# Kernel optimization log

Hardware: AMD Instinct MI355X
Metric: run time of the kernel (lower is better)

## Reference

```python
import jax, jax.numpy as jnp
import numpy as np

N = 65536      # n query/support points
NN = 34        # neighbors per point
K = 15         # kernel points
IN_F = 64
OUT_F = 64
RADIUS = 2.5
KP_EXTENT_CFG = 1.0
DENSITY = 5.0
EXTENT = KP_EXTENT_CFG * RADIUS / DENSITY  # effective KP_extent = 0.5
BN_EPS = 1e-6
LRELU_SLOPE = 0.1
POINT_DIM = 4  # modulated=True -> 3 offset dims + 1 modulation per kernel point


def make_kernel_points():
    # Deterministic stand-in for the precomputed kernel dispositions loaded
    # from disk in KPConv (fixed='center': first point at origin). Points lie
    # inside a ball of radius 1.5 * extent.
    rng = np.random.RandomState(42)
    kp = rng.normal(size=(K, 3))
    kp /= np.linalg.norm(kp, axis=1, keepdims=True)
    kp *= rng.uniform(0.3, 1.0, size=(K, 1))
    kp[0] = 0.0
    return jnp.asarray(kp * (1.5 * EXTENT), dtype=jnp.float32)


def setup_inputs() -> dict:
    key = jax.random.key(0)
    ks = jax.random.split(key, 8)
    query_points = jax.random.uniform(ks[0], (N, 3), dtype=jnp.float32)
    support_points = jax.random.uniform(ks[1], (N, 3), dtype=jnp.float32)
    neighbors_indices = jax.random.randint(ks[2], (N, NN), 0, N, dtype=jnp.int32)
    features = jax.random.normal(ks[3], (N, IN_F), dtype=jnp.float32)
    # weight_variable: truncated normal with std sqrt(2/size[-1])
    weight = jax.random.truncated_normal(ks[4], -2.0, 2.0, (K, IN_F, OUT_F), jnp.float32) * np.sqrt(2.0 / OUT_F)
    off_dim = POINT_DIM * K
    offset_weight = jax.random.truncated_normal(ks[5], -2.0, 2.0, (K, IN_F, off_dim), jnp.float32) * np.sqrt(2.0 / off_dim)
    offset_bias = jnp.zeros((off_dim,), jnp.float32)
    bn_gamma = jnp.ones((OUT_F,), jnp.float32)
    bn_beta = jnp.zeros((OUT_F,), jnp.float32)
    kernel_points = make_kernel_points()
    return dict(query_points=query_points, support_points=support_points,
                neighbors_indices=neighbors_indices, features=features,
                weight=weight, offset_weight=offset_weight, offset_bias=offset_bias,
                bn_gamma=bn_gamma, bn_beta=bn_beta, kernel_points=kernel_points)


def _influence(sq_dist):
    # KP_influence='linear': relu(1 - d / extent)
    return jax.nn.relu(1.0 - jnp.sqrt(sq_dist) / EXTENT)


def reference(query_points, support_points, neighbors_indices, features,
              weight, offset_weight, offset_bias, bn_gamma, bn_beta, kernel_points):
    n = query_points.shape[0]
    # Shadow point (far away) / shadow feature (zeros) appended at index n0
    supp_pad = jnp.concatenate([support_points, jnp.full((1, 3), 1e6, jnp.float32)], 0)
    feat_pad = jnp.concatenate([features, jnp.zeros((1, IN_F), jnp.float32)], 0)

    neigh_pts = supp_pad[neighbors_indices] - query_points[:, None, :]   # [n,nn,3]
    neigh_feats = feat_pad[neighbors_indices]                            # [n,nn,in]

    # ---- rigid KPConv producing per-point offsets (+ modulations) ----
    sq0 = jnp.sum((neigh_pts[:, :, None, :] - kernel_points[None, None]) ** 2, -1)  # [n,nn,K]
    w0 = _influence(sq0)
    wf0 = jnp.einsum('nak,nac->nkc', w0, neigh_feats)                    # [n,K,in]
    f0 = jnp.einsum('nkc,kcd->nd', wf0, offset_weight) + offset_bias     # [n,4K]
    offsets = f0[:, :3 * K].reshape(n, K, 3) * EXTENT                    # rescale to layer extent
    modulations = 2.0 * jax.nn.sigmoid(f0[:, 3 * K:])                    # [n,K]

    # ---- deformable KPConv ----
    def_kp = kernel_points[None] + offsets                               # [n,K,3]
    sq = jnp.sum((neigh_pts[:, :, None, :] - def_kp[:, None, :, :]) ** 2, -1)  # [n,nn,K]
    w = _influence(sq)                                                   # aggregation_mode='sum'
    wf = jnp.einsum('nak,nac->nkc', w, neigh_feats) * modulations[:, :, None]
    x = jnp.einsum('nkc,kco->no', wf, weight)                            # [n,out]

    # BatchNorm1d (training-mode batch stats, eps=1e-6) + LeakyReLU(0.1)
    mean = x.mean(0)
    var = x.var(0)
    x = (x - mean) * jax.lax.rsqrt(var + BN_EPS) * bn_gamma + bn_beta
    return jnp.where(x >= 0, x, LRELU_SLOPE * x)
```

## Files before the change

kernel.cpp:

```cpp
#include <hip/hip_runtime.h>
#include <math.h>

#define NPTS 65536

using half8   = __attribute__((ext_vector_type(8))) _Float16;
using half4   = __attribute__((ext_vector_type(4))) _Float16;
using floatx4 = __attribute__((ext_vector_type(4))) float;

__global__ __launch_bounds__(256) void k_prep(
    const float* __restrict__ ow, const float* __restrict__ w,
    const float* __restrict__ feat,
    _Float16* __restrict__ owt, _Float16* __restrict__ wt,
    _Float16* __restrict__ featH, float* __restrict__ stats)
{
  int b = blockIdx.x;
  if (b < 64) {
    __shared__ float tile[256][9];
    int mat = b >> 5, bb = b & 31;
    int kcb = bb & 3, db = bb >> 2;
    int t = threadIdx.x;
    int kc = kcb * 256 + t;
    int c = kc >> 4, k = kc & 15;
    const float* src = mat ? w : ow;
    int dmax = mat ? 64 : 60;
    #pragma unroll
    for (int di = 0; di < 8; ++di) {
      int d = db * 8 + di;
      float v = 0.f;
      if (k < 15 && d < dmax) v = src[(k * 64 + c) * dmax + d];
      tile[t][di] = v;
    }
    __syncthreads();
    _Float16* dst = mat ? wt : owt;
    int k2 = t >> 5, lo = t & 31;
    #pragma unroll
    for (int di = 0; di < 8; ++di) {
      int d = db * 8 + di;
      int wv = d >> 4, mm = d & 15;
      dst[((wv * 4 + kcb) * 8 + k2) * 512 + mm * 32 + lo] = (_Float16)tile[t][di];
    }
    if (b == 0 && t < 128) stats[t] = 0.f;
  } else {
    int j = (b - 64) * 256 + threadIdx.x;
    float4 f = ((const float4*)feat)[j];
    half4 h = {(_Float16)f.x, (_Float16)f.y, (_Float16)f.z, (_Float16)f.w};
    ((half4*)featH)[j] = h;
  }
}

__global__ __launch_bounds__(256, 4) void k_fused(
    const float* __restrict__ query, const float* __restrict__ support,
    const int* __restrict__ nidx, const _Float16* __restrict__ featH,
    const float* __restrict__ kpts, const float* __restrict__ obias,
    const _Float16* __restrict__ owt, const _Float16* __restrict__ wt,
    float* __restrict__ outx, float* __restrict__ stats)
{
  __shared__ float                  npx[16][34], npy[16][34], npz[16][34];
  __shared__ unsigned short         sidx[16][34];
  __shared__ __align__(16) _Float16 fT[4][64 * 32];
  __shared__ unsigned int           fx2s[16][64];
  __shared__ __align__(16) _Float16 wfh[16 * 264];
  __shared__ float                  dk[16][60];

  const int tid  = threadIdx.x;
  const int wave = tid >> 6, lane = tid & 63;
  const int quad = lane >> 4, mm = lane & 15;
  const int base = blockIdx.x * 16;
  _Float16* fTw = fT[wave];
  unsigned int* fTw32 = (unsigned int*)fTw;
  const floatx4 fz = {0.f, 0.f, 0.f, 0.f};
  const int me = (mm < 15) ? mm : 14;
  const int mmw = (mm & 6) | ((mm & 1) << 3) | ((mm >> 3) & 1);

  for (int s = tid; s < 544; s += 256) {
    int pt = s / 34, a = s - pt * 34;
    int n = base + pt;
    int id = nidx[n * 34 + a];
    npx[pt][a] = support[id * 3 + 0] - query[n * 3 + 0];
    npy[pt][a] = support[id * 3 + 1] - query[n * 3 + 1];
    npz[pt][a] = support[id * 3 + 2] - query[n * 3 + 2];
    sidx[pt][a] = (unsigned short)id;
  }
  __syncthreads();

  if (tid < 128) {
    int pt = tid >> 3, ch = tid & 7;
    int i0 = (int)sidx[pt][32], i1 = (int)sidx[pt][33];
    uint4 g0 = *(const uint4*)(featH + i0 * 64 + ch * 8);
    uint4 g1 = *(const uint4*)(featH + i1 * 64 + ch * 8);
    const uint* p0 = (const uint*)&g0;
    const uint* p1 = (const uint*)&g1;
    #pragma unroll
    for (int cc = 0; cc < 8; ++cc) {
      uint v = __builtin_amdgcn_perm(p1[cc >> 1], p0[cc >> 1],
                                     (cc & 1) ? 0x07060302u : 0x05040100u);
      fx2s[pt][ch * 8 + cc] = v;
    }
  }
  __syncthreads();

  auto load_g = [&](int pl, uint4* g0, uint4* g1) {
    #pragma unroll
    for (int it = 0; it < 2; ++it) {
      int task = it * 64 + lane;
      int rp = task >> 3, ch = task & 7;
      int i0 = (int)sidx[pl][2 * rp], i1 = (int)sidx[pl][2 * rp + 1];
      g0[it] = *(const uint4*)(featH + i0 * 64 + ch * 8);
      g1[it] = *(const uint4*)(featH + i1 * 64 + ch * 8);
    }
  };
  auto transpose_g = [&](const uint4* g0, const uint4* g1) {
    #pragma unroll
    for (int it = 0; it < 2; ++it) {
      int task = it * 64 + lane;
      int rp = task >> 3, ch = task & 7;
      int chunk = rp >> 2, o = rp & 3;
      const uint* p0 = (const uint*)&g0[it];
      const uint* p1 = (const uint*)&g1[it];
      #pragma unroll
      for (int cc = 0; cc < 8; ++cc) {
        int c  = ch * 8 + cc;
        int fc = (c & 0x36) | ((c & 1) << 3) | ((c >> 3) & 1);
        int pc = chunk ^ ((ch ^ cc) & 3);
        uint v = __builtin_amdgcn_perm(p1[cc >> 1], p0[cc >> 1],
                                       (cc & 1) ? 0x07060302u : 0x05040100u);
        fTw32[fc * 16 + pc * 4 + o] = v;
      }
    }
  };

  auto conv_point = [&](int pl, float kx, float ky, float kz, float modme,
                        half4* hq3) {
    half8 a0;
    #pragma unroll
    for (int j = 0; j < 8; ++j) {
      int a = quad * 8 + j;
      float dx = npx[pl][a] - kx, dy = npy[pl][a] - ky, dz = npz[pl][a] - kz;
      float wv = 1.f - 2.f * sqrtf(dx * dx + dy * dy + dz * dz);
      a0[j] = (_Float16)(fmaxf(wv, 0.f) * modme);
    }
    float dx = npx[pl][32] - kx, dy = npy[pl][32] - ky, dz = npz[pl][32] - kz;
    float w32 = fmaxf(1.f - 2.f * sqrtf(dx * dx + dy * dy + dz * dz), 0.f) * modme;
    dx = npx[pl][33] - kx; dy = npy[pl][33] - ky; dz = npz[pl][33] - kz;
    float w33 = fmaxf(1.f - 2.f * sqrtf(dx * dx + dy * dy + dz * dz), 0.f) * modme;
    half8 a2 = {};
    a2[0] = (_Float16)((quad == 0) ? w32 : 0.f);
    a2[1] = (_Float16)((quad == 0) ? w33 : 0.f);
    #pragma unroll
    for (int ct = 0; ct < 4; ++ct) {
      int c  = ct * 16 + mmw;
      int pc = quad ^ (((c >> 3) ^ c) & 3);
      half8 b = *(const half8*)(fTw + (ct * 16 + mm) * 32 + pc * 8);
      floatx4 acc = __builtin_amdgcn_mfma_f32_16x16x32_f16(a0, b, fz, 0, 0, 0);
      uint fp = fx2s[pl][c];
      half8 b2 = {};
      b2[0] = __builtin_bit_cast(_Float16, (unsigned short)(fp & 0xffffu));
      b2[1] = __builtin_bit_cast(_Float16, (unsigned short)(fp >> 16));
      acc = __builtin_amdgcn_mfma_f32_16x16x32_f16(a2, b2, acc, 0, 0, 0);
      half4 h = {(_Float16)acc[0], (_Float16)acc[1],
                 (_Float16)acc[2], (_Float16)acc[3]};
      if (ct == 0) *(half4*)(wfh + pl * 264 + mmw * 16 + quad * 4) = h;
      else         hq3[ct - 1] = h;
    }
  };

  auto write_hold = [&](const half4 (*hq)[3], int idx) {
    #pragma unroll
    for (int pp = 0; pp < 4; ++pp)
      *(half4*)(wfh + (wave * 4 + pp) * 264 + mmw * 16 + quad * 4) = hq[pp][idx];
  };

  auto gemm_q = [&](const _Float16* bmat, int p, floatx4& A, floatx4& B) {
    const _Float16* brow = bmat + ((wave * 4 + p) * 8) * 512 + mm * 32 + quad * 8;
    const _Float16* arow = wfh + mm * 264;
    __builtin_amdgcn_s_setprio(1);
    #pragma unroll
    for (int k2 = 0; k2 < 8; ++k2) {
      half8 af = *(const half8*)(arow + k2 * 32 + quad * 8);
      half8 bf = *(const half8*)(brow + k2 * 512);
      if (k2 & 1) B = __builtin_amdgcn_mfma_f32_16x16x32_f16(af, bf, B, 0, 0, 0);
      else        A = __builtin_amdgcn_mfma_f32_16x16x32_f16(af, bf, A, 0, 0, 0);
    }
    __builtin_amdgcn_s_setprio(0);
  };

  uint4 G0[2], G1[2];
  half4 hq[4][3];
  const float k0x = kpts[me * 3 + 0], k0y = kpts[me * 3 + 1], k0z = kpts[me * 3 + 2];

  {
    load_g(wave * 4, G0, G1);
    #pragma unroll
    for (int pp = 0; pp < 4; ++pp) {
      int pl = wave * 4 + pp;
      transpose_g(G0, G1);
      if (pp < 3) load_g(pl + 1, G0, G1);
      conv_point(pl, k0x, k0y, k0z, 1.f, hq[pp]);
    }
  }
  load_g(wave * 4, G0, G1);
  __syncthreads();

  {
    floatx4 A = fz, B = fz;
    gemm_q(owt, 0, A, B);
    __syncthreads(); write_hold(hq, 0); __syncthreads();
    gemm_q(owt, 1, A, B);
    __syncthreads(); write_hold(hq, 1); __syncthreads();
    gemm_q(owt, 2, A, B);
    __syncthreads(); write_hold(hq, 2); __syncthreads();
    gemm_q(owt, 3, A, B);
    int d = wave * 16 + mm;
    float bv = (d < 60) ? obias[d] : 0.f;
    float kv = (d < 45) ? kpts[d] : 0.f;
    #pragma unroll
    for (int r = 0; r < 4; ++r) {
      int pt = quad * 4 + r;
      float v = A[r] + B[r] + bv;
      if (d < 60)
        dk[pt][d] = (d < 45) ? (kv + 0.5f * v)
                             : (2.f / (1.f + expf(-v)));
    }
  }
  __syncthreads();

  #pragma unroll
  for (int pp = 0; pp < 4; ++pp) {
    int pl = wave * 4 + pp;
    float kx = dk[pl][me * 3 + 0], ky = dk[pl][me * 3 + 1], kz = dk[pl][me * 3 + 2];
    float modme = dk[pl][45 + me];
    transpose_g(G0, G1);
    if (pp < 3) load_g(pl + 1, G0, G1);
    conv_point(pl, kx, ky, kz, modme, hq[pp]);
  }
  __syncthreads();

  {
    floatx4 A = fz, B = fz;
    gemm_q(wt, 0, A, B);
    __syncthreads(); write_hold(hq, 0); __syncthreads();
    gemm_q(wt, 1, A, B);
    __syncthreads(); write_hold(hq, 1); __syncthreads();
    gemm_q(wt, 2, A, B);
    __syncthreads(); write_hold(hq, 2); __syncthreads();
    gemm_q(wt, 3, A, B);
    int d = wave * 16 + mm;
    float s1 = 0.f, s2 = 0.f;
    #pragma unroll
    for (int r = 0; r < 4; ++r) {
      float v = A[r] + B[r];
      outx[(base + quad * 4 + r) * 64 + d] = v;
      s1 += v; s2 += v * v;
    }
    s1 += __shfl_xor(s1, 16); s2 += __shfl_xor(s2, 16);
    s1 += __shfl_xor(s1, 32); s2 += __shfl_xor(s2, 32);
    if (lane < 16) {
      atomicAdd(&stats[d], s1);
      atomicAdd(&stats[64 + d], s2);
    }
  }
}

__global__ __launch_bounds__(256) void k_norm(
    float* __restrict__ x, const float* __restrict__ stats,
    const float* __restrict__ gamma, const float* __restrict__ beta)
{
  const int i = blockIdx.x * 256 + threadIdx.x;
  float4 v = ((float4*)x)[i];
  const int c0 = (i * 4) & 63;
  float o[4] = {v.x, v.y, v.z, v.w};
  #pragma unroll
  for (int j = 0; j < 4; ++j) {
    int c = c0 + j;
    float mean = stats[c] * (1.f / NPTS);
    float var  = stats[64 + c] * (1.f / NPTS) - mean * mean;
    float s = rsqrtf(var + 1e-6f) * gamma[c];
    float y = (o[j] - mean) * s + beta[c];
    o[j] = (y >= 0.f) ? y : 0.1f * y;
  }
  float4 rv = {o[0], o[1], o[2], o[3]};
  ((float4*)x)[i] = rv;
}

extern "C" void kernel_launch(void* const* d_in, const int* in_sizes, int n_in,
                              void* d_out, int out_size, void* d_ws, size_t ws_size,
                              hipStream_t stream)
{
  const float* query   = (const float*)d_in[0];
  const float* support = (const float*)d_in[1];
  const int*   nidx    = (const int*)d_in[2];
  const float* feat    = (const float*)d_in[3];
  const float* weight  = (const float*)d_in[4];
  const float* oweight = (const float*)d_in[5];
  const float* obias   = (const float*)d_in[6];
  const float* gamma   = (const float*)d_in[7];
  const float* beta    = (const float*)d_in[8];
  const float* kpts    = (const float*)d_in[9];
  float* x = (float*)d_out;

  char* ws = (char*)d_ws;
  _Float16* featH = (_Float16*)ws;
  _Float16* owt   = (_Float16*)(ws + 8388608);
  _Float16* wt    = (_Float16*)(ws + 8519680);
  float*    stats = (float*)(ws + 8650752);

  k_prep<<<4160, 256, 0, stream>>>(oweight, weight, feat, owt, wt, featH, stats);
  k_fused<<<4096, 256, 0, stream>>>(query, support, nidx, featH, kpts, obias,
                                    owt, wt, x, stats);
  k_norm<<<4096, 256, 0, stream>>>(x, stats, gamma, beta);
}
```

Measured before the change: 249.7 us.

## Coarsen prep and norm grids, stage kernel points in LDS, raise conv priority

The feature-to-half conversion and the norm kernel now process eight float4s per thread, so their grids shrink from 4096 blocks to 512, and the norm kernel computes the per-channel scale and shift once per thread. The fused kernel stages the kernel points in shared memory and reads them from LDS inside the loop instead of from global memory once up front. The MFMA section of conv_point is wrapped in s_setprio. The aim is to cut block-launch and per-element stats overhead in the small kernels, at the cost of fewer waves for hiding memory latency.

New measurement: 252.4 us. No clear change (+1.1%).

```diff
diff --git a/kernel.cpp b/kernel.cpp
--- a/kernel.cpp
+++ b/kernel.cpp
@@ -41,10 +41,14 @@
     }
     if (b == 0 && t < 128) stats[t] = 0.f;
   } else {
-    int j = (b - 64) * 256 + threadIdx.x;
-    float4 f = ((const float4*)feat)[j];
-    half4 h = {(_Float16)f.x, (_Float16)f.y, (_Float16)f.z, (_Float16)f.w};
-    ((half4*)featH)[j] = h;
+    int bb = b - 64;
+    #pragma unroll
+    for (int it = 0; it < 8; ++it) {
+      int j = (bb * 8 + it) * 256 + threadIdx.x;
+      float4 f = ((const float4*)feat)[j];
+      half4 h = {(_Float16)f.x, (_Float16)f.y, (_Float16)f.z, (_Float16)f.w};
+      ((half4*)featH)[j] = h;
+    }
   }
 }
 
@@ -61,6 +65,7 @@
   __shared__ unsigned int           fx2s[16][64];
   __shared__ __align__(16) _Float16 wfh[16 * 264];
   __shared__ float                  dk[16][60];
+  __shared__ float                  k0s[48];
 
   const int tid  = threadIdx.x;
   const int wave = tid >> 6, lane = tid & 63;
@@ -72,6 +77,7 @@
   const int me = (mm < 15) ? mm : 14;
   const int mmw = (mm & 6) | ((mm & 1) << 3) | ((mm >> 3) & 1);
 
+  if (tid < 45) k0s[tid] = kpts[tid];
   for (int s = tid; s < 544; s += 256) {
     int pt = s / 34, a = s - pt * 34;
     int n = base + pt;
@@ -146,6 +152,7 @@
     half8 a2 = {};
     a2[0] = (_Float16)((quad == 0) ? w32 : 0.f);
     a2[1] = (_Float16)((quad == 0) ? w33 : 0.f);
+    __builtin_amdgcn_s_setprio(1);
     #pragma unroll
     for (int ct = 0; ct < 4; ++ct) {
       int c  = ct * 16 + mmw;
@@ -162,6 +169,7 @@
       if (ct == 0) *(half4*)(wfh + pl * 264 + mmw * 16 + quad * 4) = h;
       else         hq3[ct - 1] = h;
     }
+    __builtin_amdgcn_s_setprio(0);
   };
 
   auto write_hold = [&](const half4 (*hq)[3], int idx) {
@@ -186,16 +194,16 @@
 
   uint4 G0[2], G1[2];
   half4 hq[4][3];
-  const float k0x = kpts[me * 3 + 0], k0y = kpts[me * 3 + 1], k0z = kpts[me * 3 + 2];
 
   {
     load_g(wave * 4, G0, G1);
     #pragma unroll
     for (int pp = 0; pp < 4; ++pp) {
       int pl = wave * 4 + pp;
+      float kx = k0s[me * 3 + 0], ky = k0s[me * 3 + 1], kz = k0s[me * 3 + 2];
       transpose_g(G0, G1);
       if (pp < 3) load_g(pl + 1, G0, G1);
-      conv_point(pl, k0x, k0y, k0z, 1.f, hq[pp]);
+      conv_point(pl, kx, ky, kz, 1.f, hq[pp]);
     }
   }
   load_g(wave * 4, G0, G1);
@@ -265,21 +273,29 @@
     float* __restrict__ x, const float* __restrict__ stats,
     const float* __restrict__ gamma, const float* __restrict__ beta)
 {
-  const int i = blockIdx.x * 256 + threadIdx.x;
-  float4 v = ((float4*)x)[i];
-  const int c0 = (i * 4) & 63;
-  float o[4] = {v.x, v.y, v.z, v.w};
+  const int c0 = (threadIdx.x * 4) & 63;
+  float mean[4], sc[4], bt[4];
   #pragma unroll
   for (int j = 0; j < 4; ++j) {
     int c = c0 + j;
-    float mean = stats[c] * (1.f / NPTS);
-    float var  = stats[64 + c] * (1.f / NPTS) - mean * mean;
-    float s = rsqrtf(var + 1e-6f) * gamma[c];
-    float y = (o[j] - mean) * s + beta[c];
-    o[j] = (y >= 0.f) ? y : 0.1f * y;
-  }
-  float4 rv = {o[0], o[1], o[2], o[3]};
-  ((float4*)x)[i] = rv;
+    mean[j] = stats[c] * (1.f / NPTS);
+    float var = stats[64 + c] * (1.f / NPTS) - mean[j] * mean[j];
+    sc[j] = rsqrtf(var + 1e-6f) * gamma[c];
+    bt[j] = beta[c];
+  }
+  #pragma unroll
+  for (int it = 0; it < 8; ++it) {
+    int i = (blockIdx.x * 8 + it) * 256 + threadIdx.x;
+    float4 v = ((float4*)x)[i];
+    float o[4] = {v.x, v.y, v.z, v.w};
+    #pragma unroll
+    for (int j = 0; j < 4; ++j) {
+      float y = (o[j] - mean[j]) * sc[j] + bt[j];
+      o[j] = (y >= 0.f) ? y : 0.1f * y;
+    }
+    float4 rv = {o[0], o[1], o[2], o[3]};
+    ((float4*)x)[i] = rv;
+  }
 }
 
 extern "C" void kernel_launch(void* const* d_in, const int* in_sizes, int n_in,
@@ -304,8 +320,8 @@
   _Float16* wt    = (_Float16*)(ws + 8519680);
   float*    stats = (float*)(ws + 8650752);
 
-  k_prep<<<4160, 256, 0, stream>>>(oweight, weight, feat, owt, wt, featH, stats);
+  k_prep<<<576, 256, 0, stream>>>(oweight, weight, feat, owt, wt, featH, stats);
   k_fused<<<4096, 256, 0, stream>>>(query, support, nidx, featH, kpts, obias,
                                     owt, wt, x, stats);
-  k_norm<<<4096, 256, 0, stream>>>(x, stats, gamma, beta);
+  k_norm<<<512, 256, 0, stream>>>(x, stats, gamma, beta);
 }
```
